# Optimization experiments

Hardware: AMD Instinct MI355X
Metric: run time of the kernel (lower is better)

Reference implementation:

```python
import jax, jax.numpy as jnp
import numpy as np

N_NODES = 100000
N_EDGES = 1600000
IN_DIM = 128
HID = 32
HEADS = 4
OUT_DIM = 40
NEG_SLOPE = 0.2
BN_EPS = 1e-5


def setup_inputs() -> dict:
    key = jax.random.key(0)
    ks = jax.random.split(key, 13)
    x = jax.random.normal(ks[0], (N_NODES, IN_DIM), jnp.float32)
    edge_index = jax.random.randint(ks[1], (2, N_EDGES), 0, N_NODES, dtype=jnp.int32)
    s0 = 1.0 / np.sqrt(IN_DIM)
    s1 = 1.0 / np.sqrt(HEADS * HID)
    return {
        "x": x,
        "edge_index": edge_index,
        # layer 0: GATConv(IN_DIM -> HID, HEADS heads, concat)
        "W0": jax.random.normal(ks[2], (IN_DIM, HEADS * HID), jnp.float32) * s0,
        "a_src0": jax.random.normal(ks[3], (HEADS, HID), jnp.float32) * s0,
        "a_dst0": jax.random.normal(ks[4], (HEADS, HID), jnp.float32) * s0,
        "b0": jnp.zeros((HEADS * HID,), jnp.float32),
        # BatchNorm1d(HEADS*HID)
        "gamma0": jnp.ones((HEADS * HID,), jnp.float32),
        "beta0": jnp.zeros((HEADS * HID,), jnp.float32),
        # layer 1: GATConv(HEADS*HID -> OUT_DIM, 1 head, mean)
        "W1": jax.random.normal(ks[5], (HEADS * HID, OUT_DIM), jnp.float32) * s1,
        "a_src1": jax.random.normal(ks[6], (1, OUT_DIM), jnp.float32) * s1,
        "a_dst1": jax.random.normal(ks[7], (1, OUT_DIM), jnp.float32) * s1,
        "b1": jnp.zeros((OUT_DIM,), jnp.float32),
    }


def gat_conv(x, src, dst, n_nodes, W, a_src, a_dst, b, heads, concat):
    # linear transform: [N, H, C]
    h = (x @ W).reshape(n_nodes, heads, -1)
    # per-node attention logits [N, H]
    alpha_src = (h * a_src).sum(-1)
    alpha_dst = (h * a_dst).sum(-1)
    # per-edge raw attention [E, H]
    e = jax.nn.leaky_relu(alpha_src[src] + alpha_dst[dst], NEG_SLOPE)
    # softmax over incoming edges of each destination node
    m = jax.ops.segment_max(e, dst, num_segments=n_nodes)  # self-loops -> no empty segment
    ex = jnp.exp(e - m[dst])
    den = jax.ops.segment_sum(ex, dst, num_segments=n_nodes)
    # weighted scatter-aggregate of messages [E, H, C] -> [N, H, C]
    out = jax.ops.segment_sum(ex[:, :, None] * h[src], dst, num_segments=n_nodes)
    out = out / den[:, :, None]
    out = out.reshape(n_nodes, -1) if concat else out.mean(axis=1)
    return out + b


def batch_norm(x, gamma, beta):
    mu = x.mean(axis=0)
    var = x.var(axis=0)
    return (x - mu) * jax.lax.rsqrt(var + BN_EPS) * gamma + beta


def reference(x, edge_index, W0, a_src0, a_dst0, b0, gamma0, beta0,
              W1, a_src1, a_dst1, b1):
    n = x.shape[0]
    loop = jnp.arange(n, dtype=edge_index.dtype)
    src = jnp.concatenate([edge_index[0], loop])  # add self-loops (PyG default)
    dst = jnp.concatenate([edge_index[1], loop])
    # layer 0: GATConv -> BN -> ELU (dropout p=0 / eval -> identity)
    h = gat_conv(x, src, dst, n, W0, a_src0, a_dst0, b0, HEADS, True)
    h = jax.nn.elu(batch_norm(h, gamma0, beta0))
    # layer 1: GATConv, 1 head, mean aggregation, no BN/act
    out = gat_conv(h, src, dst, n, W1, a_src1, a_dst1, b1, 1, False)
    return out
```

## Files before the change

kernel.cpp:

```cpp
#include <hip/hip_runtime.h>
#include <hip/hip_bf16.h>
#include <math.h>

#define NN   100000
#define EE   1600000
#define ETOT (NN + EE)
#define IND  128
#define HD   128
#define OD   40
#define NEG  0.2f
#define BNEPS 1e-5f
#define NBKT 16

#define NGEMM ((NN + 63) / 64)
#define NDEG  ((ETOT / 8 + 255) / 256)
#define NTRIPLE 831
#define NFUSED (NTRIPLE * 3)

typedef __attribute__((ext_vector_type(8))) short bf16x8;
typedef __attribute__((ext_vector_type(4))) float f32x4;

__device__ __forceinline__ float lrelu(float x) { return x > 0.f ? x : NEG * x; }

__device__ __forceinline__ unsigned pack_bf16(float a, float b) {
  unsigned ua = __float_as_uint(a), ub = __float_as_uint(b);
  ua = (ua + 0x7fffu + ((ua >> 16) & 1u)) >> 16;
  ub = (ub + 0x7fffu + ((ub >> 16) & 1u)) >> 16;
  return ua | (ub << 16);
}
__device__ __forceinline__ float bf16_lo(unsigned v) { return __uint_as_float(v << 16); }
__device__ __forceinline__ float bf16_hi(unsigned v) { return __uint_as_float(v & 0xffff0000u); }

__global__ __launch_bounds__(256) void fused0_kernel(const float* __restrict__ x,
                                                     const float* __restrict__ W0,
                                                     const float* __restrict__ a_src0,
                                                     const float* __restrict__ a_dst0,
                                                     unsigned* __restrict__ h0b,
                                                     float* __restrict__ asrc0,
                                                     float* __restrict__ adst0,
                                                     const int* __restrict__ ei,
                                                     int* __restrict__ deg,
                                                     int* __restrict__ rank) {
  __shared__ __align__(16) unsigned As[64][68];
  __shared__ __align__(16) unsigned Wt[128][68];
  int bid = blockIdx.x;
  int trip = bid / 3, rem = bid - trip * 3;
  int t = threadIdx.x;

  if (rem == 2) {
    int i8 = (trip * 256 + t) * 8;
    if (i8 >= ETOT) return;
    int4 dA, dB;
    if (i8 < EE) {
      dA = *(const int4*)&ei[EE + i8];
      dB = *(const int4*)&ei[EE + i8 + 4];
    } else {
      int b = i8 - EE;
      dA = make_int4(b, b + 1, b + 2, b + 3);
      dB = make_int4(b + 4, b + 5, b + 6, b + 7);
    }
    int4 rA, rB;
    rA.x = atomicAdd(&deg[dA.x], 1);
    rA.y = atomicAdd(&deg[dA.y], 1);
    rA.z = atomicAdd(&deg[dA.z], 1);
    rA.w = atomicAdd(&deg[dA.w], 1);
    rB.x = atomicAdd(&deg[dB.x], 1);
    rB.y = atomicAdd(&deg[dB.y], 1);
    rB.z = atomicAdd(&deg[dB.z], 1);
    rB.w = atomicAdd(&deg[dB.w], 1);
    *(int4*)&rank[i8] = rA;
    *(int4*)&rank[i8 + 4] = rB;
    return;
  }

  int gb = trip * 2 + rem;
  if (gb >= NGEMM) return;
  int rowbase = gb * 64;

  for (int idx = t; idx < 128 * 64; idx += 256) {
    int kp = idx >> 7, n = idx & 127;
    float lo = W0[(size_t)(2 * kp) * 128 + n];
    float hi = W0[(size_t)(2 * kp + 1) * 128 + n];
    Wt[n][kp] = pack_bf16(lo, hi);
  }
  for (int idx = t; idx < 64 * 64; idx += 256) {
    int row = idx >> 6, kp = idx & 63;
    int r = rowbase + row;
    int rc = r < NN ? r : NN - 1;
    float2 v = *(const float2*)&x[(size_t)rc * 128 + kp * 2];
    As[row][kp] = pack_bf16(v.x, v.y);
  }
  __syncthreads();

  int lane = t & 63, w = t >> 6;
  int mrow = lane & 15, g = lane >> 4;
  f32x4 acc[8];
#pragma unroll
  for (int nt = 0; nt < 8; nt++) acc[nt] = (f32x4){0.f, 0.f, 0.f, 0.f};
#pragma unroll
  for (int ks = 0; ks < 4; ks++) {
    bf16x8 a = *(const bf16x8*)&As[w * 16 + mrow][ks * 16 + g * 4];
#pragma unroll
    for (int nt = 0; nt < 8; nt++) {
      bf16x8 b = *(const bf16x8*)&Wt[nt * 16 + mrow][ks * 16 + g * 4];
      acc[nt] = __builtin_amdgcn_mfma_f32_16x16x32_bf16(a, b, acc[nt], 0, 0, 0);
    }
  }
  int col = lane & 15;
  float as_[8], ad_[8];
#pragma unroll
  for (int nt = 0; nt < 8; nt++) {
    as_[nt] = a_src0[nt * 16 + col];
    ad_[nt] = a_dst0[nt * 16 + col];
  }
#pragma unroll
  for (int reg = 0; reg < 4; reg++) {
    int r = rowbase + w * 16 + g * 4 + reg;
    bool rok = r < NN;
    float hs0 = acc[0][reg] * as_[0] + acc[1][reg] * as_[1];
    float hs1 = acc[2][reg] * as_[2] + acc[3][reg] * as_[3];
    float hs2 = acc[4][reg] * as_[4] + acc[5][reg] * as_[5];
    float hs3 = acc[6][reg] * as_[6] + acc[7][reg] * as_[7];
    float hd0 = acc[0][reg] * ad_[0] + acc[1][reg] * ad_[1];
    float hd1 = acc[2][reg] * ad_[2] + acc[3][reg] * ad_[3];
    float hd2 = acc[4][reg] * ad_[4] + acc[5][reg] * ad_[5];
    float hd3 = acc[6][reg] * ad_[6] + acc[7][reg] * ad_[7];
#pragma unroll
    for (int mk = 1; mk < 16; mk <<= 1) {
      hs0 += __shfl_xor(hs0, mk); hs1 += __shfl_xor(hs1, mk);
      hs2 += __shfl_xor(hs2, mk); hs3 += __shfl_xor(hs3, mk);
      hd0 += __shfl_xor(hd0, mk); hd1 += __shfl_xor(hd1, mk);
      hd2 += __shfl_xor(hd2, mk); hd3 += __shfl_xor(hd3, mk);
    }
    if ((lane & 15) == 0 && rok) {
      asrc0[r * 4 + 0] = hs0; asrc0[r * 4 + 1] = hs1;
      asrc0[r * 4 + 2] = hs2; asrc0[r * 4 + 3] = hs3;
      adst0[r * 4 + 0] = hd0; adst0[r * 4 + 1] = hd1;
      adst0[r * 4 + 2] = hd2; adst0[r * 4 + 3] = hd3;
    }
#pragma unroll
    for (int nt = 0; nt < 8; nt++) {
      float v = acc[nt][reg];
      float nv = __shfl_xor(v, 1);
      if (!(col & 1) && rok) h0b[(size_t)r * 64 + nt * 8 + (col >> 1)] = pack_bf16(v, nv);
    }
  }
}

__global__ __launch_bounds__(256) void scanA_kernel(const int* __restrict__ deg,
                                                    int* __restrict__ scanned,
                                                    int* __restrict__ blocksums) {
  __shared__ int s[256];
  int t = threadIdx.x;
  int i = blockIdx.x * 256 + t;
  int v = (i < NN) ? deg[i] : 0;
  s[t] = v;
  __syncthreads();
  for (int off = 1; off < 256; off <<= 1) {
    int add = (t >= off) ? s[t - off] : 0;
    __syncthreads();
    s[t] += add;
    __syncthreads();
  }
  if (i < NN) scanned[i] = s[t];
  if (t == 255) blocksums[blockIdx.x] = s[255];
}

__global__ __launch_bounds__(512) void scanB_kernel(int* __restrict__ blocksums, int NB) {
  __shared__ int s[512];
  int t = threadIdx.x;
  int v = (t < NB) ? blocksums[t] : 0;
  s[t] = v;
  __syncthreads();
  for (int off = 1; off < 512; off <<= 1) {
    int add = (t >= off) ? s[t - off] : 0;
    __syncthreads();
    s[t] += add;
    __syncthreads();
  }
  if (t < NB) blocksums[t] = s[t] - v;
}

__global__ __launch_bounds__(256) void scanC_kernel(const int* __restrict__ scanned,
                                                    const int* __restrict__ deg,
                                                    const int* __restrict__ blocksums,
                                                    int* __restrict__ rowptr) {
  int i = blockIdx.x * 256 + threadIdx.x;
  if (i < NN) rowptr[i] = blocksums[blockIdx.x] + scanned[i] - deg[i];
  if (i == 0) rowptr[NN] = ETOT;
}

__global__ void scatter_kernel(const int* __restrict__ ei, const int* __restrict__ rowptr,
                               const int* __restrict__ rank, int* __restrict__ csr_src) {
  int i8 = (blockIdx.x * blockDim.x + threadIdx.x) * 8;
  if (i8 >= ETOT) return;
  int4 sA, dA, sB, dB;
  if (i8 < EE) {
    sA = *(const int4*)&ei[i8];
    sB = *(const int4*)&ei[i8 + 4];
    dA = *(const int4*)&ei[EE + i8];
    dB = *(const int4*)&ei[EE + i8 + 4];
  } else {
    int b = i8 - EE;
    sA = make_int4(b, b + 1, b + 2, b + 3);
    sB = make_int4(b + 4, b + 5, b + 6, b + 7);
    dA = sA; dB = sB;
  }
  int4 rA = *(const int4*)&rank[i8];
  int4 rB = *(const int4*)&rank[i8 + 4];
  int p0 = rowptr[dA.x] + rA.x;
  int p1 = rowptr[dA.y] + rA.y;
  int p2 = rowptr[dA.z] + rA.z;
  int p3 = rowptr[dA.w] + rA.w;
  int p4 = rowptr[dB.x] + rB.x;
  int p5 = rowptr[dB.y] + rB.y;
  int p6 = rowptr[dB.z] + rB.z;
  int p7 = rowptr[dB.w] + rB.w;
  csr_src[p0] = sA.x;
  csr_src[p1] = sA.y;
  csr_src[p2] = sA.z;
  csr_src[p3] = sA.w;
  csr_src[p4] = sB.x;
  csr_src[p5] = sB.y;
  csr_src[p6] = sB.z;
  csr_src[p7] = sB.w;
}

__global__ __launch_bounds__(256) void agg0_kernel(const int* __restrict__ csr_src,
                                                   const int* __restrict__ rowptr,
                                                   const float* __restrict__ asrc0,
                                                   const float* __restrict__ adst0,
                                                   const unsigned* __restrict__ h0b,
                                                   const float* __restrict__ b0,
                                                   unsigned* __restrict__ agg0b,
                                                   float* __restrict__ bnsumB,
                                                   float* __restrict__ bnsqB) {
  __shared__ float ws[16][4][17];
  __shared__ int   ss[16][16];
  __shared__ float Lsum[4][16][8], Lsq[4][16][8];
  int t = threadIdx.x;
  int grp = t >> 4;
  int p   = t & 15;
  int n = blockIdx.x * 16 + grp;
  int start = rowptr[n], end = rowptr[n + 1];
  float4 ad = *(const float4*)&adst0[(size_t)n * 4];
  int head = p >> 2;
  float a0 = 0.f, a1 = 0.f, a2 = 0.f, a3 = 0.f, a4 = 0.f, a5 = 0.f, a6 = 0.f, a7 = 0.f;
  float d0 = 0.f, d1 = 0.f, d2 = 0.f, d3 = 0.f;

  for (int base = start; base < end; base += 16) {
    int cnt = min(16, end - base);
    if (p < cnt) {
      int s = csr_src[base + p];
      float4 as = *(const float4*)&asrc0[(size_t)s * 4];
      float w0 = __expf(lrelu(as.x + ad.x));
      float w1 = __expf(lrelu(as.y + ad.y));
      float w2 = __expf(lrelu(as.z + ad.z));
      float w3 = __expf(lrelu(as.w + ad.w));
      d0 += w0; d1 += w1; d2 += w2; d3 += w3;
      ss[grp][p] = s;
      ws[grp][0][p] = w0;
      ws[grp][1][p] = w1;
      ws[grp][2][p] = w2;
      ws[grp][3][p] = w3;
    }
    __builtin_amdgcn_wave_barrier();
    for (int eb = 0; eb < cnt; eb += 4) {
      int e0 = eb, e1 = eb + 1, e2 = eb + 2, e3 = eb + 3;
      float w0 = ws[grp][head][e0];
      float w1 = (e1 < cnt) ? ws[grp][head][e1] : 0.f;
      float w2 = (e2 < cnt) ? ws[grp][head][e2] : 0.f;
      float w3 = (e3 < cnt) ? ws[grp][head][e3] : 0.f;
      int s0 = ss[grp][e0];
      int s1 = ss[grp][(e1 < cnt) ? e1 : e0];
      int s2 = ss[grp][(e2 < cnt) ? e2 : e0];
      int s3 = ss[grp][(e3 < cnt) ? e3 : e0];
      uint4 h0v = *(const uint4*)&h0b[(size_t)s0 * 64 + p * 4];
      uint4 h1v = *(const uint4*)&h0b[(size_t)s1 * 64 + p * 4];
      uint4 h2v = *(const uint4*)&h0b[(size_t)s2 * 64 + p * 4];
      uint4 h3v = *(const uint4*)&h0b[(size_t)s3 * 64 + p * 4];
      a0 += w0 * bf16_lo(h0v.x); a1 += w0 * bf16_hi(h0v.x);
      a2 += w0 * bf16_lo(h0v.y); a3 += w0 * bf16_hi(h0v.y);
      a4 += w0 * bf16_lo(h0v.z); a5 += w0 * bf16_hi(h0v.z);
      a6 += w0 * bf16_lo(h0v.w); a7 += w0 * bf16_hi(h0v.w);
      a0 += w1 * bf16_lo(h1v.x); a1 += w1 * bf16_hi(h1v.x);
      a2 += w1 * bf16_lo(h1v.y); a3 += w1 * bf16_hi(h1v.y);
      a4 += w1 * bf16_lo(h1v.z); a5 += w1 * bf16_hi(h1v.z);
      a6 += w1 * bf16_lo(h1v.w); a7 += w1 * bf16_hi(h1v.w);
      a0 += w2 * bf16_lo(h2v.x); a1 += w2 * bf16_hi(h2v.x);
      a2 += w2 * bf16_lo(h2v.y); a3 += w2 * bf16_hi(h2v.y);
      a4 += w2 * bf16_lo(h2v.z); a5 += w2 * bf16_hi(h2v.z);
      a6 += w2 * bf16_lo(h2v.w); a7 += w2 * bf16_hi(h2v.w);
      a0 += w3 * bf16_lo(h3v.x); a1 += w3 * bf16_hi(h3v.x);
      a2 += w3 * bf16_lo(h3v.y); a3 += w3 * bf16_hi(h3v.y);
      a4 += w3 * bf16_lo(h3v.z); a5 += w3 * bf16_hi(h3v.z);
      a6 += w3 * bf16_lo(h3v.w); a7 += w3 * bf16_hi(h3v.w);
    }
    __builtin_amdgcn_wave_barrier();
  }
#pragma unroll
  for (int mk = 1; mk < 16; mk <<= 1) {
    d0 += __shfl_xor(d0, mk);
    d1 += __shfl_xor(d1, mk);
    d2 += __shfl_xor(d2, mk);
    d3 += __shfl_xor(d3, mk);
  }
  float dh = head == 0 ? d0 : head == 1 ? d1 : head == 2 ? d2 : d3;
  float rd = 1.f / dh;
  int c = p * 8;
  float4 b1v = *(const float4*)&b0[c];
  float4 b2v = *(const float4*)&b0[c + 4];
  float o0 = a0 * rd + b1v.x, o1 = a1 * rd + b1v.y;
  float o2 = a2 * rd + b1v.z, o3 = a3 * rd + b1v.w;
  float o4 = a4 * rd + b2v.x, o5 = a5 * rd + b2v.y;
  float o6 = a6 * rd + b2v.z, o7 = a7 * rd + b2v.w;
  uint4 o;
  o.x = pack_bf16(o0, o1);
  o.y = pack_bf16(o2, o3);
  o.z = pack_bf16(o4, o5);
  o.w = pack_bf16(o6, o7);
  *(uint4*)&agg0b[(size_t)n * 64 + p * 4] = o;

  float s0 = o0, s1 = o1, s2 = o2, s3 = o3, s4 = o4, s5 = o5, s6 = o6, s7 = o7;
  float q0 = o0 * o0, q1 = o1 * o1, q2 = o2 * o2, q3 = o3 * o3;
  float q4 = o4 * o4, q5 = o5 * o5, q6 = o6 * o6, q7 = o7 * o7;
#pragma unroll
  for (int mk = 16; mk < 64; mk <<= 1) {
    s0 += __shfl_xor(s0, mk); s1 += __shfl_xor(s1, mk);
    s2 += __shfl_xor(s2, mk); s3 += __shfl_xor(s3, mk);
    s4 += __shfl_xor(s4, mk); s5 += __shfl_xor(s5, mk);
    s6 += __shfl_xor(s6, mk); s7 += __shfl_xor(s7, mk);
    q0 += __shfl_xor(q0, mk); q1 += __shfl_xor(q1, mk);
    q2 += __shfl_xor(q2, mk); q3 += __shfl_xor(q3, mk);
    q4 += __shfl_xor(q4, mk); q5 += __shfl_xor(q5, mk);
    q6 += __shfl_xor(q6, mk); q7 += __shfl_xor(q7, mk);
  }
  int lane = t & 63, wv = t >> 6;
  if (lane < 16) {
    Lsum[wv][lane][0] = s0; Lsum[wv][lane][1] = s1;
    Lsum[wv][lane][2] = s2; Lsum[wv][lane][3] = s3;
    Lsum[wv][lane][4] = s4; Lsum[wv][lane][5] = s5;
    Lsum[wv][lane][6] = s6; Lsum[wv][lane][7] = s7;
    Lsq[wv][lane][0] = q0; Lsq[wv][lane][1] = q1;
    Lsq[wv][lane][2] = q2; Lsq[wv][lane][3] = q3;
    Lsq[wv][lane][4] = q4; Lsq[wv][lane][5] = q5;
    Lsq[wv][lane][6] = q6; Lsq[wv][lane][7] = q7;
  }
  __syncthreads();
  if (t < 128) {
    int pp = t >> 3, jj = t & 7;
    float s = Lsum[0][pp][jj] + Lsum[1][pp][jj] + Lsum[2][pp][jj] + Lsum[3][pp][jj];
    float q = Lsq[0][pp][jj] + Lsq[1][pp][jj] + Lsq[2][pp][jj] + Lsq[3][pp][jj];
    int bkt = blockIdx.x & (NBKT - 1);
    atomicAdd(&bnsumB[bkt * 128 + t], s);
    atomicAdd(&bnsqB[bkt * 128 + t], q);
  }
}

__global__ __launch_bounds__(256) void gemm1_kernel(const unsigned* __restrict__ agg0b,
                                                    const float* __restrict__ bnsumB,
                                                    const float* __restrict__ bnsqB,
                                                    const float* __restrict__ gamma,
                                                    const float* __restrict__ beta,
                                                    const float* __restrict__ W1,
                                                    const float* __restrict__ a_src1,
                                                    const float* __restrict__ a_dst1,
                                                    unsigned* __restrict__ h1b,
                                                    float* __restrict__ asrc1,
                                                    float* __restrict__ adst1) {
  __shared__ __align__(16) unsigned As[64][68];
  __shared__ __align__(16) unsigned Wt[48][68];
  __shared__ float bnsc[128], bnsh[128];
  int t = threadIdx.x;
  int rowbase = blockIdx.x * 64;

  if (t < 128) {
    float s = 0.f, q = 0.f;
#pragma unroll
    for (int k = 0; k < NBKT; k++) {
      s += bnsumB[k * 128 + t];
      q += bnsqB[k * 128 + t];
    }
    float mu = s / (float)NN;
    float var = q / (float)NN - mu * mu;
    float sc = gamma[t] / sqrtf(var + BNEPS);
    bnsc[t] = sc;
    bnsh[t] = beta[t] - mu * sc;
  }
  for (int idx = t; idx < 48 * 64; idx += 256) {
    int c = idx >> 6, kp = idx & 63;
    float lo = (c < OD) ? W1[(size_t)(2 * kp) * OD + c] : 0.f;
    float hi = (c < OD) ? W1[(size_t)(2 * kp + 1) * OD + c] : 0.f;
    Wt[c][kp] = pack_bf16(lo, hi);
  }
  __syncthreads();
  for (int idx = t; idx < 64 * 16; idx += 256) {
    int row = idx >> 4, c4 = idx & 15;
    int r = rowbase + row;
    int rc = r < NN ? r : NN - 1;
    int k = c4 * 8;
    uint4 hv = *(const uint4*)&agg0b[(size_t)rc * 64 + c4 * 4];
    float y0 = bf16_lo(hv.x) * bnsc[k + 0] + bnsh[k + 0];
    float y1 = bf16_hi(hv.x) * bnsc[k + 1] + bnsh[k + 1];
    float y2 = bf16_lo(hv.y) * bnsc[k + 2] + bnsh[k + 2];
    float y3 = bf16_hi(hv.y) * bnsc[k + 3] + bnsh[k + 3];
    float y4 = bf16_lo(hv.z) * bnsc[k + 4] + bnsh[k + 4];
    float y5 = bf16_hi(hv.z) * bnsc[k + 5] + bnsh[k + 5];
    float y6 = bf16_lo(hv.w) * bnsc[k + 6] + bnsh[k + 6];
    float y7 = bf16_hi(hv.w) * bnsc[k + 7] + bnsh[k + 7];
    y0 = y0 > 0.f ? y0 : expm1f(y0);
    y1 = y1 > 0.f ? y1 : expm1f(y1);
    y2 = y2 > 0.f ? y2 : expm1f(y2);
    y3 = y3 > 0.f ? y3 : expm1f(y3);
    y4 = y4 > 0.f ? y4 : expm1f(y4);
    y5 = y5 > 0.f ? y5 : expm1f(y5);
    y6 = y6 > 0.f ? y6 : expm1f(y6);
    y7 = y7 > 0.f ? y7 : expm1f(y7);
    As[row][c4 * 4 + 0] = pack_bf16(y0, y1);
    As[row][c4 * 4 + 1] = pack_bf16(y2, y3);
    As[row][c4 * 4 + 2] = pack_bf16(y4, y5);
    As[row][c4 * 4 + 3] = pack_bf16(y6, y7);
  }
  __syncthreads();

  int lane = t & 63, w = t >> 6;
  int mrow = lane & 15, g = lane >> 4;
  f32x4 acc0 = {0.f, 0.f, 0.f, 0.f};
  f32x4 acc1 = {0.f, 0.f, 0.f, 0.f};
  f32x4 acc2 = {0.f, 0.f, 0.f, 0.f};
#pragma unroll
  for (int ks = 0; ks < 4; ks++) {
    bf16x8 a = *(const bf16x8*)&As[w * 16 + mrow][ks * 16 + g * 4];
    bf16x8 b0v = *(const bf16x8*)&Wt[mrow][ks * 16 + g * 4];
    bf16x8 b1v = *(const bf16x8*)&Wt[16 + mrow][ks * 16 + g * 4];
    bf16x8 b2v = *(const bf16x8*)&Wt[32 + mrow][ks * 16 + g * 4];
    acc0 = __builtin_amdgcn_mfma_f32_16x16x32_bf16(a, b0v, acc0, 0, 0, 0);
    acc1 = __builtin_amdgcn_mfma_f32_16x16x32_bf16(a, b1v, acc1, 0, 0, 0);
    acc2 = __builtin_amdgcn_mfma_f32_16x16x32_bf16(a, b2v, acc2, 0, 0, 0);
  }
  int col = lane & 15;
  float as0 = (col < OD)      ? a_src1[col]      : 0.f;
  float as1 = (16 + col < OD) ? a_src1[16 + col] : 0.f;
  float as2 = (32 + col < OD) ? a_src1[32 + col] : 0.f;
  float ad0 = (col < OD)      ? a_dst1[col]      : 0.f;
  float ad1 = (16 + col < OD) ? a_dst1[16 + col] : 0.f;
  float ad2 = (32 + col < OD) ? a_dst1[32 + col] : 0.f;
#pragma unroll
  for (int reg = 0; reg < 4; reg++) {
    int r = rowbase + w * 16 + g * 4 + reg;
    float v0 = acc0[reg], v1 = acc1[reg], v2 = acc2[reg];
    float ps = v0 * as0 + v1 * as1 + v2 * as2;
    float pd = v0 * ad0 + v1 * ad1 + v2 * ad2;
#pragma unroll
    for (int mk = 1; mk < 16; mk <<= 1) { ps += __shfl_xor(ps, mk); pd += __shfl_xor(pd, mk); }
    bool rok = r < NN;
    if ((lane & 15) == 0 && rok) { asrc1[r] = ps; adst1[r] = pd; }
    float n0 = __shfl_xor(v0, 1), n1 = __shfl_xor(v1, 1), n2 = __shfl_xor(v2, 1);
    if (!(col & 1) && rok) {
      h1b[(size_t)r * 20 + ((col) >> 1)]      = pack_bf16(v0, n0);
      h1b[(size_t)r * 20 + ((16 + col) >> 1)] = pack_bf16(v1, n1);
      if (32 + col < OD) h1b[(size_t)r * 20 + ((32 + col) >> 1)] = pack_bf16(v2, n2);
    }
  }
}

__global__ __launch_bounds__(256) void agg1_kernel(const int* __restrict__ csr_src,
                                                   const int* __restrict__ rowptr,
                                                   const float* __restrict__ asrc1,
                                                   const float* __restrict__ adst1,
                                                   const unsigned* __restrict__ h1b,
                                                   const float* __restrict__ b1,
                                                   float* __restrict__ out) {
  __shared__ float ws[4][64];
  __shared__ int   ss[4][64];
  int t = threadIdx.x;
  int lane = t & 63, wv = t >> 6;
  int n = blockIdx.x * 4 + wv;
  if (n >= NN) return;
  int start = rowptr[n], end = rowptr[n + 1];
  float ad = adst1[n];
  int esub = lane / 10;
  int c2   = lane - esub * 10;
  float dsum = 0.f;
  float acc0 = 0.f, acc1 = 0.f, acc2 = 0.f, acc3 = 0.f;
  for (int base = start; base < end; base += 64) {
    int cnt = min(64, end - base);
    if (lane < cnt) {
      int s = csr_src[base + lane];
      float w = __expf(lrelu(asrc1[s] + ad));
      dsum += w;
      ss[wv][lane] = s;
      ws[wv][lane] = w;
    }
    __builtin_amdgcn_wave_barrier();
    if (lane < 60) {
      int e = esub;
      for (; e + 18 < cnt; e += 24) {
        int s0 = ss[wv][e], s1 = ss[wv][e + 6], s2 = ss[wv][e + 12], s3 = ss[wv][e + 18];
        uint2 u0 = *(const uint2*)&h1b[(size_t)s0 * 20 + c2 * 2];
        uint2 u1 = *(const uint2*)&h1b[(size_t)s1 * 20 + c2 * 2];
        uint2 u2 = *(const uint2*)&h1b[(size_t)s2 * 20 + c2 * 2];
        uint2 u3 = *(const uint2*)&h1b[(size_t)s3 * 20 + c2 * 2];
        float w0 = ws[wv][e], w1 = ws[wv][e + 6], w2 = ws[wv][e + 12], w3 = ws[wv][e + 18];
        acc0 += w0 * bf16_lo(u0.x); acc1 += w0 * bf16_hi(u0.x);
        acc2 += w0 * bf16_lo(u0.y); acc3 += w0 * bf16_hi(u0.y);
        acc0 += w1 * bf16_lo(u1.x); acc1 += w1 * bf16_hi(u1.x);
        acc2 += w1 * bf16_lo(u1.y); acc3 += w1 * bf16_hi(u1.y);
        acc0 += w2 * bf16_lo(u2.x); acc1 += w2 * bf16_hi(u2.x);
        acc2 += w2 * bf16_lo(u2.y); acc3 += w2 * bf16_hi(u2.y);
        acc0 += w3 * bf16_lo(u3.x); acc1 += w3 * bf16_hi(u3.x);
        acc2 += w3 * bf16_lo(u3.y); acc3 += w3 * bf16_hi(u3.y);
      }
      for (; e < cnt; e += 6) {
        int s = ss[wv][e];
        float w = ws[wv][e];
        uint2 u = *(const uint2*)&h1b[(size_t)s * 20 + c2 * 2];
        acc0 += w * bf16_lo(u.x); acc1 += w * bf16_hi(u.x);
        acc2 += w * bf16_lo(u.y); acc3 += w * bf16_hi(u.y);
      }
    }
    __builtin_amdgcn_wave_barrier();
  }
#pragma unroll
  for (int mk = 1; mk < 64; mk <<= 1) dsum += __shfl_xor(dsum, mk);
  float rd = 1.f / dsum;
  float p01 = __shfl(acc0, lane + 10), p02 = __shfl(acc0, lane + 20);
  float p03 = __shfl(acc0, lane + 30), p04 = __shfl(acc0, lane + 40);
  float p05 = __shfl(acc0, lane + 50);
  float p11 = __shfl(acc1, lane + 10), p12 = __shfl(acc1, lane + 20);
  float p13 = __shfl(acc1, lane + 30), p14 = __shfl(acc1, lane + 40);
  float p15 = __shfl(acc1, lane + 50);
  float p21 = __shfl(acc2, lane + 10), p22 = __shfl(acc2, lane + 20);
  float p23 = __shfl(acc2, lane + 30), p24 = __shfl(acc2, lane + 40);
  float p25 = __shfl(acc2, lane + 50);
  float p31 = __shfl(acc3, lane + 10), p32 = __shfl(acc3, lane + 20);
  float p33 = __shfl(acc3, lane + 30), p34 = __shfl(acc3, lane + 40);
  float p35 = __shfl(acc3, lane + 50);
  if (lane < 10) {
    float t0 = acc0 + p01 + p02 + p03 + p04 + p05;
    float t1 = acc1 + p11 + p12 + p13 + p14 + p15;
    float t2 = acc2 + p21 + p22 + p23 + p24 + p25;
    float t3 = acc3 + p31 + p32 + p33 + p34 + p35;
    float4 bv = *(const float4*)&b1[lane * 4];
    float4 o;
    o.x = t0 * rd + bv.x;
    o.y = t1 * rd + bv.y;
    o.z = t2 * rd + bv.z;
    o.w = t3 * rd + bv.w;
    *(float4*)&out[(size_t)n * 40 + lane * 4] = o;
  }
}

extern "C" void kernel_launch(void* const* d_in, const int* in_sizes, int n_in,
                              void* d_out, int out_size, void* d_ws, size_t ws_size,
                              hipStream_t stream) {
  const float* x       = (const float*)d_in[0];
  const int*   ei      = (const int*)d_in[1];
  const float* W0      = (const float*)d_in[2];
  const float* a_src0  = (const float*)d_in[3];
  const float* a_dst0  = (const float*)d_in[4];
  const float* b0      = (const float*)d_in[5];
  const float* gamma0  = (const float*)d_in[6];
  const float* beta0   = (const float*)d_in[7];
  const float* W1      = (const float*)d_in[8];
  const float* a_src1  = (const float*)d_in[9];
  const float* a_dst1  = (const float*)d_in[10];
  const float* b1      = (const float*)d_in[11];
  float* out = (float*)d_out;

  char* ws = (char*)d_ws;
  size_t off = 0;
  auto alloc = [&](size_t bytes) {
    void* p = ws + off;
    off += (bytes + 255) & ~(size_t)255;
    return p;
  };
  int*   deg      = (int*)alloc((size_t)NN * 4);
  float* bnsumB   = (float*)alloc(NBKT * 128 * 4);
  float* bnsqB    = (float*)alloc(NBKT * 128 * 4);
  unsigned* h0b   = (unsigned*)alloc((size_t)NN * 64 * 4);
  unsigned* agg0b = (unsigned*)alloc((size_t)NN * 64 * 4);
  unsigned* h1b   = (unsigned*)alloc((size_t)NN * 20 * 4);
  float* asrc0    = (float*)alloc((size_t)NN * 4 * 4);
  float* adst0    = (float*)alloc((size_t)NN * 4 * 4);
  float* asrc1    = (float*)alloc((size_t)NN * 4);
  float* adst1    = (float*)alloc((size_t)NN * 4);
  int*   rowptr   = (int*)alloc((size_t)(NN + 1) * 4);
  int*   scanned  = (int*)alloc((size_t)NN * 4);
  int*   csr      = (int*)alloc((size_t)ETOT * 4);
  int*   rank     = (int*)alloc((size_t)ETOT * 4);
  int*   bsums    = (int*)alloc(512 * 4);
  (void)ws_size; (void)in_sizes; (void)n_in; (void)out_size;

  size_t zbytes = (char*)(bnsqB + NBKT * 128) - (char*)deg;
  hipMemsetAsync(deg, 0, zbytes, stream);

  const int NB = (NN + 255) / 256;
  const int e8grid = (ETOT / 8 + 255) / 256;

  fused0_kernel<<<NFUSED, 256, 0, stream>>>(x, W0, a_src0, a_dst0, h0b, asrc0, adst0,
                                            ei, deg, rank);
  scanA_kernel<<<NB, 256, 0, stream>>>(deg, scanned, bsums);
  scanB_kernel<<<1, 512, 0, stream>>>(bsums, NB);
  scanC_kernel<<<NB, 256, 0, stream>>>(scanned, deg, bsums, rowptr);
  scatter_kernel<<<e8grid, 256, 0, stream>>>(ei, rowptr, rank, csr);
  agg0_kernel<<<NN / 16, 256, 0, stream>>>(csr, rowptr, asrc0, adst0, h0b, b0, agg0b,
                                           bnsumB, bnsqB);
  gemm1_kernel<<<(NN + 63) / 64, 256, 0, stream>>>(agg0b, bnsumB, bnsqB, gamma0, beta0,
                                                   W1, a_src1, a_dst1, h1b, asrc1, adst1);
  agg1_kernel<<<(NN + 3) / 4, 256, 0, stream>>>(csr, rowptr, asrc1, adst1, h1b, b1, out);
}
```

Baseline: 280.5 us.

## Replace three-kernel scan with single-pass decoupled look-back scan

Merges the three-kernel exclusive scan over node degrees into one kernel that uses decoupled look-back. Each tile publishes its aggregate and inclusive prefix through flagged status words, which are zeroed by the existing memset. This removes two kernel launches and the intermediate scanned and blocksums arrays. In exchange it depends on tiles being scheduled in order and on spin-waiting with atomics, and the look-back is serial in thread 0.

```diff
diff --git a/kernel.cpp b/kernel.cpp
--- a/kernel.cpp
+++ b/kernel.cpp
@@ -147,12 +147,14 @@
   }
 }
 
-__global__ __launch_bounds__(256) void scanA_kernel(const int* __restrict__ deg,
-                                                    int* __restrict__ scanned,
-                                                    int* __restrict__ blocksums) {
+__global__ __launch_bounds__(256) void scanS_kernel(const int* __restrict__ deg,
+                                                    unsigned* __restrict__ tstat,
+                                                    int* __restrict__ rowptr) {
   __shared__ int s[256];
+  __shared__ int exc_sh;
+  int tile = blockIdx.x;
   int t = threadIdx.x;
-  int i = blockIdx.x * 256 + t;
+  int i = tile * 256 + t;
   int v = (i < NN) ? deg[i] : 0;
   s[t] = v;
   __syncthreads();
@@ -162,32 +164,31 @@
     s[t] += add;
     __syncthreads();
   }
-  if (i < NN) scanned[i] = s[t];
-  if (t == 255) blocksums[blockIdx.x] = s[255];
-}
-
-__global__ __launch_bounds__(512) void scanB_kernel(int* __restrict__ blocksums, int NB) {
-  __shared__ int s[512];
-  int t = threadIdx.x;
-  int v = (t < NB) ? blocksums[t] : 0;
-  s[t] = v;
+  int incl = s[t];
+  int total = s[255];
+  if (t == 0) {
+    int exc = 0;
+    if (tile == 0) {
+      atomicExch(&tstat[0], (2u << 30) | (unsigned)total);
+    } else {
+      atomicExch(&tstat[tile], (1u << 30) | (unsigned)total);
+      int pt = tile - 1;
+      while (pt >= 0) {
+        unsigned st = atomicAdd(&tstat[pt], 0u);
+        unsigned flag = st >> 30;
+        if (flag == 0u) continue;
+        exc += (int)(st & 0x3FFFFFFFu);
+        if (flag == 2u) break;
+        pt--;
+      }
+      atomicExch(&tstat[tile], (2u << 30) | (unsigned)(exc + total));
+    }
+    exc_sh = exc;
+  }
   __syncthreads();
-  for (int off = 1; off < 512; off <<= 1) {
-    int add = (t >= off) ? s[t - off] : 0;
-    __syncthreads();
-    s[t] += add;
-    __syncthreads();
-  }
-  if (t < NB) blocksums[t] = s[t] - v;
-}
-
-__global__ __launch_bounds__(256) void scanC_kernel(const int* __restrict__ scanned,
-                                                    const int* __restrict__ deg,
-                                                    const int* __restrict__ blocksums,
-                                                    int* __restrict__ rowptr) {
-  int i = blockIdx.x * 256 + threadIdx.x;
-  if (i < NN) rowptr[i] = blocksums[blockIdx.x] + scanned[i] - deg[i];
-  if (i == 0) rowptr[NN] = ETOT;
+  int exc = exc_sh;
+  if (i < NN) rowptr[i] = exc + incl - v;
+  if (i == NN - 1) rowptr[NN] = exc + incl;
 }
 
 __global__ void scatter_kernel(const int* __restrict__ ei, const int* __restrict__ rowptr,
@@ -575,24 +576,23 @@
     off += (bytes + 255) & ~(size_t)255;
     return p;
   };
-  int*   deg      = (int*)alloc((size_t)NN * 4);
-  float* bnsumB   = (float*)alloc(NBKT * 128 * 4);
-  float* bnsqB    = (float*)alloc(NBKT * 128 * 4);
-  unsigned* h0b   = (unsigned*)alloc((size_t)NN * 64 * 4);
-  unsigned* agg0b = (unsigned*)alloc((size_t)NN * 64 * 4);
-  unsigned* h1b   = (unsigned*)alloc((size_t)NN * 20 * 4);
-  float* asrc0    = (float*)alloc((size_t)NN * 4 * 4);
-  float* adst0    = (float*)alloc((size_t)NN * 4 * 4);
-  float* asrc1    = (float*)alloc((size_t)NN * 4);
-  float* adst1    = (float*)alloc((size_t)NN * 4);
-  int*   rowptr   = (int*)alloc((size_t)(NN + 1) * 4);
-  int*   scanned  = (int*)alloc((size_t)NN * 4);
-  int*   csr      = (int*)alloc((size_t)ETOT * 4);
-  int*   rank     = (int*)alloc((size_t)ETOT * 4);
-  int*   bsums    = (int*)alloc(512 * 4);
+  int*      deg    = (int*)alloc((size_t)NN * 4);
+  float*    bnsumB = (float*)alloc(NBKT * 128 * 4);
+  float*    bnsqB  = (float*)alloc(NBKT * 128 * 4);
+  unsigned* tstat  = (unsigned*)alloc(512 * 4);
+  unsigned* h0b    = (unsigned*)alloc((size_t)NN * 64 * 4);
+  unsigned* agg0b  = (unsigned*)alloc((size_t)NN * 64 * 4);
+  unsigned* h1b    = (unsigned*)alloc((size_t)NN * 20 * 4);
+  float* asrc0     = (float*)alloc((size_t)NN * 4 * 4);
+  float* adst0     = (float*)alloc((size_t)NN * 4 * 4);
+  float* asrc1     = (float*)alloc((size_t)NN * 4);
+  float* adst1     = (float*)alloc((size_t)NN * 4);
+  int*   rowptr    = (int*)alloc((size_t)(NN + 1) * 4);
+  int*   csr       = (int*)alloc((size_t)ETOT * 4);
+  int*   rank      = (int*)alloc((size_t)ETOT * 4);
   (void)ws_size; (void)in_sizes; (void)n_in; (void)out_size;
 
-  size_t zbytes = (char*)(bnsqB + NBKT * 128) - (char*)deg;
+  size_t zbytes = (char*)(tstat + 512) - (char*)deg;
   hipMemsetAsync(deg, 0, zbytes, stream);
 
   const int NB = (NN + 255) / 256;
@@ -600,9 +600,7 @@
 
   fused0_kernel<<<NFUSED, 256, 0, stream>>>(x, W0, a_src0, a_dst0, h0b, asrc0, adst0,
                                             ei, deg, rank);
-  scanA_kernel<<<NB, 256, 0, stream>>>(deg, scanned, bsums);
-  scanB_kernel<<<1, 512, 0, stream>>>(bsums, NB);
-  scanC_kernel<<<NB, 256, 0, stream>>>(scanned, deg, bsums, rowptr);
+  scanS_kernel<<<NB, 256, 0, stream>>>(deg, tstat, rowptr);
   scatter_kernel<<<e8grid, 256, 0, stream>>>(ei, rowptr, rank, csr);
   agg0_kernel<<<NN / 16, 256, 0, stream>>>(csr, rowptr, asrc0, adst0, h0b, b0, agg0b,
                                            bnsumB, bnsqB);
```

Measured after the change: 289.7 us. 1.03x slower.
